# Optimization experiments

Measured on AMD Instinct MI355X. Metric: run time of the kernel, lower is better.

The kernel has to match this reference:

```python
import jax, jax.numpy as jnp
import numpy as np

E = 1024  # embedding_dim
H = 64    # head_size

def setup_inputs() -> dict:
    key = jax.random.key(0)
    k1, k2, k3, k4 = jax.random.split(key, 4)
    x = jax.random.normal(k1, (4, 4096, E), dtype=jnp.float32)
    # nn.Linear(E, H, bias=False) weights have shape [H, E]; y = x @ W.T
    s = 1.0 / np.sqrt(E)
    Wq = jax.random.normal(k2, (H, E), dtype=jnp.float32) * s
    Wk = jax.random.normal(k3, (H, E), dtype=jnp.float32) * s
    Wv = jax.random.normal(k4, (H, E), dtype=jnp.float32) * s
    return {"x": x, "Wq": Wq, "Wk": Wk, "Wv": Wv}

def reference(x, Wq, Wk, Wv):
    B, T, E_ = x.shape
    q = jnp.einsum('bte,he->bth', x, Wq)
    k = jnp.einsum('bte,he->bth', x, Wk)
    v = jnp.einsum('bte,he->bth', x, Wv)
    # NOTE: original scales by sqrt(embedding_dim), not head_size
    scores = jnp.einsum('bqh,bkh->bqk', q, k) / jnp.sqrt(jnp.asarray(E_, x.dtype))
    causal = jnp.tril(jnp.ones((T, T), dtype=bool))
    scores = jnp.where(causal, scores, -jnp.inf)
    weights = jax.nn.softmax(scores, axis=-1)
    return jnp.einsum('bqk,bkh->bqh', weights, v)
```

## Files before the change

kernel.cpp:

```cpp
#include <hip/hip_runtime.h>
#include <stdint.h>

typedef __bf16 bf16x8 __attribute__((ext_vector_type(8)));
typedef float  f32x4  __attribute__((ext_vector_type(4)));

#define E_DIM 1024
#define H_DIM 64
#define T_SEQ 4096
#define B_BAT 4
#define M_TOT (B_BAT * T_SEQ)
#define NSPLIT 8

__device__ __forceinline__ uint32_t f2bf1(float f) {
    uint32_t u = __float_as_uint(f);
    return (u + 0x7FFFu + ((u >> 16) & 1u)) >> 16;
}
__device__ __forceinline__ uint32_t pk2(float lo, float hi) {
    return f2bf1(lo) | (f2bf1(hi) << 16);
}
__device__ __forceinline__ bf16x8 ldfrag(const ushort* p) {
    return __builtin_bit_cast(bf16x8, *(const uint4*)(p));
}
__device__ __forceinline__ void barrier_lgkm() {
    __builtin_amdgcn_s_waitcnt(0xC07F);
    __builtin_amdgcn_s_barrier();
}

__global__ __launch_bounds__(256) void wcvt(const float* __restrict__ Wq,
                                            const float* __restrict__ Wk,
                                            const float* __restrict__ Wv,
                                            ushort* __restrict__ Wfm) {
    int g = blockIdx.x * 256 + threadIdx.x;
    int n = g >> 7;
    int k8 = g & 127;
    const float* src = (n < 64) ? (Wq + (size_t)n * E_DIM)
                     : (n < 128) ? (Wk + (size_t)(n - 64) * E_DIM)
                     : (Wv + (size_t)(n - 128) * E_DIM);
    float sc = (n < 64) ? 0.03125f : 1.0f;
    float4 a = *(const float4*)(src + k8 * 8);
    float4 b = *(const float4*)(src + k8 * 8 + 4);
    uint4 o;
    o.x = pk2(a.x * sc, a.y * sc); o.y = pk2(a.z * sc, a.w * sc);
    o.z = pk2(b.x * sc, b.y * sc); o.w = pk2(b.z * sc, b.w * sc);
    int s = k8 >> 3, kc = (k8 >> 2) & 1, qd = k8 & 3;
    int nt = n >> 4, lm = n & 15;
    int lane = qd * 16 + lm;
    *(uint4*)(Wfm + (((size_t)(s * 12 + nt) * 2 + kc) * 64 + lane) * 8) = o;
}

__global__ __launch_bounds__(256, 3) void qkv(const float* __restrict__ x,
                                              const ushort* __restrict__ Wfm,
                                              ushort* __restrict__ Qfm,
                                              ushort* __restrict__ Kfm,
                                              ushort* __restrict__ Vfm) {
    __shared__ union {
        ushort a[2][32 * 72];
        struct { ushort c[32 * 136]; ushort vt[64 * 40]; } epi;
    } sm;
    const int tid = threadIdx.x;
    const int w = tid >> 6, l = tid & 63;
    const int lm = l & 15, qd = l >> 4;
    const int m0 = blockIdx.x * 32;

    f32x4 acc[2][3];
#pragma unroll
    for (int r2 = 0; r2 < 2; ++r2)
#pragma unroll
        for (int t = 0; t < 3; ++t) acc[r2][t] = (f32x4){0.f, 0.f, 0.f, 0.f};

    const int srow = tid >> 3, kseg = tid & 7;
    const float* xsrc = x + (size_t)(m0 + srow) * E_DIM + kseg * 8;

    {
        float4 a0 = *(const float4*)xsrc;
        float4 a1 = *(const float4*)(xsrc + 4);
        uint4 u = {pk2(a0.x, a0.y), pk2(a0.z, a0.w), pk2(a1.x, a1.y), pk2(a1.z, a1.w)};
        *(uint4*)(&sm.a[0][srow * 72 + kseg * 8]) = u;
    }
    float4 xn0 = *(const float4*)(xsrc + 64);
    float4 xn1 = *(const float4*)(xsrc + 68);
    __syncthreads();

    for (int s = 0; s < 16; ++s) {
        const int cb = s & 1, nb = cb ^ 1;
        float4 x20 = xn0, x21 = xn1;
        if (s < 14) {
            x20 = *(const float4*)(xsrc + (s + 2) * 64);
            x21 = *(const float4*)(xsrc + (s + 2) * 64 + 4);
        }
        bf16x8 wf[3][2];
#pragma unroll
        for (int t = 0; t < 3; ++t)
#pragma unroll
            for (int kc = 0; kc < 2; ++kc)
                wf[t][kc] = ldfrag(Wfm + (((size_t)(s * 12 + w * 3 + t) * 2 + kc) * 64 + l) * 8);
        bf16x8 af[2][2];
#pragma unroll
        for (int r2 = 0; r2 < 2; ++r2)
#pragma unroll
            for (int kc = 0; kc < 2; ++kc)
                af[r2][kc] = ldfrag(&sm.a[cb][(r2 * 16 + lm) * 72 + kc * 32 + qd * 8]);
#pragma unroll
        for (int t = 0; t < 3; ++t)
#pragma unroll
            for (int kc = 0; kc < 2; ++kc)
#pragma unroll
                for (int r2 = 0; r2 < 2; ++r2)
                    acc[r2][t] = __builtin_amdgcn_mfma_f32_16x16x32_bf16(af[r2][kc], wf[t][kc], acc[r2][t], 0, 0, 0);
        if (s < 15) {
            uint4 u = {pk2(xn0.x, xn0.y), pk2(xn0.z, xn0.w), pk2(xn1.x, xn1.y), pk2(xn1.z, xn1.w)};
            *(uint4*)(&sm.a[nb][srow * 72 + kseg * 8]) = u;
        }
        xn0 = x20; xn1 = x21;
        if (s < 15) barrier_lgkm();
    }
    __syncthreads();

#pragma unroll
    for (int r2 = 0; r2 < 2; ++r2)
#pragma unroll
        for (int t = 0; t < 3; ++t) {
            int gc = w * 48 + t * 16 + lm;
            int m = r2 * 16 + qd * 4;
#pragma unroll
            for (int rr = 0; rr < 4; ++rr) {
                ushort v = (ushort)f2bf1(acc[r2][t][rr]);
                if (gc < 128) sm.epi.c[(m + rr) * 136 + gc] = v;
                else          sm.epi.vt[(gc - 128) * 40 + (m + rr)] = v;
            }
        }
    __syncthreads();

    const int g16b = m0 >> 4;
    const int kt64 = m0 >> 6;
    const int tb   = (m0 >> 4) & 3;
    const int kcv  = (m0 >> 5) & 1;
#pragma unroll
    for (int ii = 0; ii < 3; ++ii) {
        int i = w + ii * 4;
        uint4 val;
        ushort* dst;
        if (i < 4) {
            int qt_l = i >> 1, kc = i & 1;
            val = *(const uint4*)(&sm.epi.c[(qt_l * 16 + lm) * 136 + kc * 32 + qd * 8]);
            dst = Qfm + (((size_t)(g16b + qt_l) * 2 + kc) * 64 + l) * 8;
        } else if (i < 8) {
            int j2 = i - 4, t_l = j2 >> 1, kc = j2 & 1;
            val = *(const uint4*)(&sm.epi.c[(t_l * 16 + lm) * 136 + 64 + kc * 32 + qd * 8]);
            dst = Kfm + (((size_t)((kt64 * 4 + tb + t_l) * 2 + kc)) * 64 + l) * 8;
        } else {
            int t = i - 8;
            val = *(const uint4*)(&sm.epi.vt[(t * 16 + lm) * 40 + qd * 8]);
            dst = Vfm + (((size_t)((kt64 * 4 + t) * 2 + kcv)) * 64 + l) * 8;
        }
        *(uint4*)dst = val;
    }
}

__global__ __launch_bounds__(256, 4) void flash(const ushort* __restrict__ Qfm,
                                                const ushort* __restrict__ Kfm,
                                                const ushort* __restrict__ Vfm,
                                                float* __restrict__ Opart,
                                                float* __restrict__ lpart) {
    __shared__ ushort plds[4][16 * 72];
    const int tid = threadIdx.x;
    const int wv = tid >> 6, l = tid & 63;
    const int lm = l & 15, qd = l >> 4;
    const int pr = blockIdx.x;
    const int bt = blockIdx.y;
    const int h  = blockIdx.z;
    ushort* myp = plds[wv];

#pragma unroll 1
    for (int half = 0; half < 2; ++half) {
        const int qt = half ? (63 - pr) : pr;
        const size_t rowg = (size_t)bt * T_SEQ + qt * 64 + wv * 16;
        const int g16 = bt * 256 + qt * 4 + wv;

        bf16x8 qf0, qf1;
        {
            const ushort* qp = Qfm + ((size_t)g16 * 2) * 512 + l * 8;
            qf0 = ldfrag(qp);
            qf1 = ldfrag(qp + 512);
        }
        f32x4 o[4];
#pragma unroll
        for (int t = 0; t < 4; ++t) o[t] = (f32x4){0.f, 0.f, 0.f, 0.f};
        float lacc = 0.f;

#pragma unroll 1
        for (int kt = h; kt <= qt; kt += NSPLIT) {
            const ushort* kb = Kfm + ((size_t)(bt * 64 + kt) * 8) * 512;
            const ushort* vb = Vfm + ((size_t)(bt * 64 + kt) * 8) * 512;
            f32x4 sf[4];
#pragma unroll
            for (int t = 0; t < 4; ++t) sf[t] = (f32x4){0.f, 0.f, 0.f, 0.f};
#pragma unroll
            for (int t = 0; t < 4; ++t) {
                bf16x8 k0 = ldfrag(kb + (t * 2 + 0) * 512 + l * 8);
                bf16x8 k1 = ldfrag(kb + (t * 2 + 1) * 512 + l * 8);
                sf[t] = __builtin_amdgcn_mfma_f32_16x16x32_bf16(k0, qf0, sf[t], 0, 0, 0);
                sf[t] = __builtin_amdgcn_mfma_f32_16x16x32_bf16(k1, qf1, sf[t], 0, 0, 0);
            }
            uint4 vu[4][2];
#pragma unroll
            for (int t = 0; t < 4; ++t) {
                vu[t][0] = *(const uint4*)(vb + (t * 2 + 0) * 512 + l * 8);
                vu[t][1] = *(const uint4*)(vb + (t * 2 + 1) * 512 + l * 8);
            }
            ushort* wp = myp + lm * 72 + qd * 4;
            if (kt != qt) {
#pragma unroll
                for (int t = 0; t < 4; ++t) {
                    float p0 = __expf(sf[t][0]), p1 = __expf(sf[t][1]);
                    float p2 = __expf(sf[t][2]), p3 = __expf(sf[t][3]);
                    lacc += (p0 + p1) + (p2 + p3);
                    *(uint2*)(wp + t * 16) = uint2{pk2(p0, p1), pk2(p2, p3)};
                }
            } else {
#pragma unroll
                for (int t = 0; t < 4; ++t) {
                    if (t < wv) {
                        float p0 = __expf(sf[t][0]), p1 = __expf(sf[t][1]);
                        float p2 = __expf(sf[t][2]), p3 = __expf(sf[t][3]);
                        lacc += (p0 + p1) + (p2 + p3);
                        *(uint2*)(wp + t * 16) = uint2{pk2(p0, p1), pk2(p2, p3)};
                    } else if (t == wv) {
                        float p[4];
#pragma unroll
                        for (int rr = 0; rr < 4; ++rr) {
                            float pe = __expf(sf[t][rr]);
                            if (qd * 4 + rr > lm) pe = 0.f;
                            lacc += pe;
                            p[rr] = pe;
                        }
                        *(uint2*)(wp + t * 16) = uint2{pk2(p[0], p[1]), pk2(p[2], p[3])};
                    } else {
                        *(uint2*)(wp + t * 16) = uint2{0u, 0u};
                    }
                }
            }
            __builtin_amdgcn_wave_barrier();
            __builtin_amdgcn_s_waitcnt(0xC07F);
            __builtin_amdgcn_wave_barrier();
            bf16x8 pf0 = ldfrag(myp + lm * 72 + qd * 8);
            bf16x8 pf1 = ldfrag(myp + lm * 72 + 32 + qd * 8);
#pragma unroll
            for (int t = 0; t < 4; ++t) {
                bf16x8 v0 = __builtin_bit_cast(bf16x8, vu[t][0]);
                bf16x8 v1 = __builtin_bit_cast(bf16x8, vu[t][1]);
                o[t] = __builtin_amdgcn_mfma_f32_16x16x32_bf16(pf0, v0, o[t], 0, 0, 0);
                o[t] = __builtin_amdgcn_mfma_f32_16x16x32_bf16(pf1, v1, o[t], 0, 0, 0);
            }
            __builtin_amdgcn_wave_barrier();
        }
        lacc += __shfl_xor(lacc, 16);
        lacc += __shfl_xor(lacc, 32);

        float* ob = Opart + ((size_t)h * M_TOT + rowg) * 64;
#pragma unroll
        for (int t = 0; t < 4; ++t)
#pragma unroll
            for (int rr = 0; rr < 4; ++rr)
                ob[(size_t)(qd * 4 + rr) * 64 + t * 16 + lm] = o[t][rr];
        if (qd == 0) lpart[(size_t)h * M_TOT + rowg + lm] = lacc;
    }
}

__global__ __launch_bounds__(256) void combine(const float* __restrict__ Opart,
                                               const float* __restrict__ lpart,
                                               float* __restrict__ out) {
    int i4 = blockIdx.x * 256 + threadIdx.x;
    size_t base = (size_t)i4 * 4;
    int row = i4 >> 4;
    float ls = 0.f;
#pragma unroll
    for (int s = 0; s < NSPLIT; ++s) ls += lpart[(size_t)s * M_TOT + row];
    const size_t SP = (size_t)M_TOT * 64;
    float4 o = {0.f, 0.f, 0.f, 0.f};
#pragma unroll
    for (int s = 0; s < NSPLIT; ++s) {
        float4 a = *(const float4*)(Opart + (size_t)s * SP + base);
        o.x += a.x; o.y += a.y; o.z += a.z; o.w += a.w;
    }
    float inv = 1.0f / ls;
    o.x *= inv; o.y *= inv; o.z *= inv; o.w *= inv;
    *(float4*)(out + base) = o;
}

extern "C" void kernel_launch(void* const* d_in, const int* in_sizes, int n_in,
                              void* d_out, int out_size, void* d_ws, size_t ws_size,
                              hipStream_t stream) {
    const float* x  = (const float*)d_in[0];
    const float* Wq = (const float*)d_in[1];
    const float* Wk = (const float*)d_in[2];
    const float* Wv = (const float*)d_in[3];
    float* out = (float*)d_out;

    char* ws = (char*)d_ws;
    ushort* Wfm = (ushort*)(ws);
    ushort* Qfm = (ushort*)(ws + 393216);
    ushort* Kfm = (ushort*)(ws + 2490368);
    ushort* Vfm = (ushort*)(ws + 4587520);
    float*  Op  = (float*) (ws + 6684672);
    float*  lp  = (float*) (ws + 6684672 + (size_t)NSPLIT * M_TOT * 64 * 4);

    wcvt<<<96, 256, 0, stream>>>(Wq, Wk, Wv, Wfm);
    qkv<<<512, 256, 0, stream>>>(x, Wfm, Qfm, Kfm, Vfm);
    flash<<<dim3(32, B_BAT, NSPLIT), 256, 0, stream>>>(Qfm, Kfm, Vfm, Op, lp);
    combine<<<1024, 256, 0, stream>>>(Op, lp, out);
}
```

Measured before the change: 139.9 us.

## Fold log2e into Q scale, use exp2, halve KV splits, deepen prefetch

The Q weight scale now includes log2(e), so the softmax can use the hardware exp2 builtin instead of __expf. The bit-manual bf16 rounding is replaced by a native __bf16 cast. The split-K count for the flash kernel drops from 8 to 4, which shrinks the partial buffers and the combine work but launches fewer blocks. The x prefetch in the QKV projection kernel deepens from two stages ahead to three.

```diff
diff --git a/kernel.cpp b/kernel.cpp
--- a/kernel.cpp
+++ b/kernel.cpp
@@ -9,14 +9,16 @@
 #define T_SEQ 4096
 #define B_BAT 4
 #define M_TOT (B_BAT * T_SEQ)
-#define NSPLIT 8
-
-__device__ __forceinline__ uint32_t f2bf1(float f) {
-    uint32_t u = __float_as_uint(f);
-    return (u + 0x7FFFu + ((u >> 16) & 1u)) >> 16;
+#define NSPLIT 4
+
+__device__ __forceinline__ ushort f2bfu(float f) {
+    return __builtin_bit_cast(ushort, (__bf16)f);
 }
 __device__ __forceinline__ uint32_t pk2(float lo, float hi) {
-    return f2bf1(lo) | (f2bf1(hi) << 16);
+    return (uint32_t)f2bfu(lo) | ((uint32_t)f2bfu(hi) << 16);
+}
+__device__ __forceinline__ float ex2(float x) {
+    return __builtin_amdgcn_exp2f(x);
 }
 __device__ __forceinline__ bf16x8 ldfrag(const ushort* p) {
     return __builtin_bit_cast(bf16x8, *(const uint4*)(p));
@@ -36,7 +38,7 @@
     const float* src = (n < 64) ? (Wq + (size_t)n * E_DIM)
                      : (n < 128) ? (Wk + (size_t)(n - 64) * E_DIM)
                      : (Wv + (size_t)(n - 128) * E_DIM);
-    float sc = (n < 64) ? 0.03125f : 1.0f;
+    float sc = (n < 64) ? 0.045084220f : 1.0f;
     float4 a = *(const float4*)(src + k8 * 8);
     float4 b = *(const float4*)(src + k8 * 8 + 4);
     uint4 o;
@@ -77,16 +79,18 @@
         uint4 u = {pk2(a0.x, a0.y), pk2(a0.z, a0.w), pk2(a1.x, a1.y), pk2(a1.z, a1.w)};
         *(uint4*)(&sm.a[0][srow * 72 + kseg * 8]) = u;
     }
-    float4 xn0 = *(const float4*)(xsrc + 64);
-    float4 xn1 = *(const float4*)(xsrc + 68);
+    float4 xa0 = *(const float4*)(xsrc + 64);
+    float4 xa1 = *(const float4*)(xsrc + 68);
+    float4 xb0 = *(const float4*)(xsrc + 128);
+    float4 xb1 = *(const float4*)(xsrc + 132);
     __syncthreads();
 
     for (int s = 0; s < 16; ++s) {
         const int cb = s & 1, nb = cb ^ 1;
-        float4 x20 = xn0, x21 = xn1;
-        if (s < 14) {
-            x20 = *(const float4*)(xsrc + (s + 2) * 64);
-            x21 = *(const float4*)(xsrc + (s + 2) * 64 + 4);
+        float4 xc0 = xa0, xc1 = xa1;
+        if (s < 13) {
+            xc0 = *(const float4*)(xsrc + (s + 3) * 64);
+            xc1 = *(const float4*)(xsrc + (s + 3) * 64 + 4);
         }
         bf16x8 wf[3][2];
 #pragma unroll
@@ -108,10 +112,10 @@
                 for (int r2 = 0; r2 < 2; ++r2)
                     acc[r2][t] = __builtin_amdgcn_mfma_f32_16x16x32_bf16(af[r2][kc], wf[t][kc], acc[r2][t], 0, 0, 0);
         if (s < 15) {
-            uint4 u = {pk2(xn0.x, xn0.y), pk2(xn0.z, xn0.w), pk2(xn1.x, xn1.y), pk2(xn1.z, xn1.w)};
+            uint4 u = {pk2(xa0.x, xa0.y), pk2(xa0.z, xa0.w), pk2(xa1.x, xa1.y), pk2(xa1.z, xa1.w)};
             *(uint4*)(&sm.a[nb][srow * 72 + kseg * 8]) = u;
         }
-        xn0 = x20; xn1 = x21;
+        xa0 = xb0; xa1 = xb1; xb0 = xc0; xb1 = xc1;
         if (s < 15) barrier_lgkm();
     }
     __syncthreads();
@@ -124,7 +128,7 @@
             int m = r2 * 16 + qd * 4;
 #pragma unroll
             for (int rr = 0; rr < 4; ++rr) {
-                ushort v = (ushort)f2bf1(acc[r2][t][rr]);
+                ushort v = f2bfu(acc[r2][t][rr]);
                 if (gc < 128) sm.epi.c[(m + rr) * 136 + gc] = v;
                 else          sm.epi.vt[(gc - 128) * 40 + (m + rr)] = v;
             }
@@ -212,8 +216,8 @@
             if (kt != qt) {
 #pragma unroll
                 for (int t = 0; t < 4; ++t) {
-                    float p0 = __expf(sf[t][0]), p1 = __expf(sf[t][1]);
-                    float p2 = __expf(sf[t][2]), p3 = __expf(sf[t][3]);
+                    float p0 = ex2(sf[t][0]), p1 = ex2(sf[t][1]);
+                    float p2 = ex2(sf[t][2]), p3 = ex2(sf[t][3]);
                     lacc += (p0 + p1) + (p2 + p3);
                     *(uint2*)(wp + t * 16) = uint2{pk2(p0, p1), pk2(p2, p3)};
                 }
@@ -221,15 +225,15 @@
 #pragma unroll
                 for (int t = 0; t < 4; ++t) {
                     if (t < wv) {
-                        float p0 = __expf(sf[t][0]), p1 = __expf(sf[t][1]);
-                        float p2 = __expf(sf[t][2]), p3 = __expf(sf[t][3]);
+                        float p0 = ex2(sf[t][0]), p1 = ex2(sf[t][1]);
+                        float p2 = ex2(sf[t][2]), p3 = ex2(sf[t][3]);
                         lacc += (p0 + p1) + (p2 + p3);
                         *(uint2*)(wp + t * 16) = uint2{pk2(p0, p1), pk2(p2, p3)};
                     } else if (t == wv) {
                         float p[4];
 #pragma unroll
                         for (int rr = 0; rr < 4; ++rr) {
-                            float pe = __expf(sf[t][rr]);
+                            float pe = ex2(sf[t][rr]);
                             if (qd * 4 + rr > lm) pe = 0.f;
                             lacc += pe;
                             p[rr] = pe;
@@ -303,7 +307,7 @@
     ushort* Kfm = (ushort*)(ws + 2490368);
     ushort* Vfm = (ushort*)(ws + 4587520);
     float*  Op  = (float*) (ws + 6684672);
-    float*  lp  = (float*) (ws + 6684672 + (size_t)NSPLIT * M_TOT * 64 * 4);
+    float*  lp  = (float*) (ws + 23461888);
 
     wcvt<<<96, 256, 0, stream>>>(Wq, Wk, Wv, Wfm);
     qkv<<<512, 256, 0, stream>>>(x, Wfm, Qfm, Kfm, Vfm);
```

New measurement: 135.2 us. 1.03x faster.
